# Optimization experiments

Measured on AMD Instinct MI355X. Metric: run time of the kernel, lower is better.

Reference implementation:

```python
import jax, jax.numpy as jnp
import numpy as np
from jax import lax

ANCHOR_NUM = 5
OUTPUT_NUM = 4  # 'reg' branch


def setup_inputs() -> dict:
    key = jax.random.key(0)
    k1, k2 = jax.random.split(key)
    detection = jax.random.normal(k1, (64, 20, 20, 256), dtype=jnp.float32)
    templates = jax.random.normal(k2, (64, 4, 4, 256 * ANCHOR_NUM * OUTPUT_NUM), dtype=jnp.float32)
    return {"detection": detection, "templates": templates}


def reference(detection, templates):
    # detection: [B, Hd, Wd, C]; templates: [B, Hk, Wk, C * O]
    # Original TF code fakes per-example-kernel conv via one big depthwise_conv2d
    # followed by reduce_sum over channel groups. Mathematically:
    #   out[b, y, x, o] = sum_{i,j,c} detection[b, y+i, x+j, c] * tmpl[b, i, j, c, o]
    # i.e. a per-example VALID cross-correlation. We express it as a vmapped conv.
    B, Hd, Wd, C = detection.shape
    _, Hk, Wk, CO = templates.shape
    O = CO // C  # anchor_num * output_num = 20
    tmpl = templates.reshape(B, Hk, Wk, C, O)

    def corr_one(det, ker):
        # det: [Hd, Wd, C], ker: [Hk, Wk, C, O] -> [Ho, Wo, O]
        out = lax.conv_general_dilated(
            det[None],  # [1, Hd, Wd, C]
            ker,        # HWIO
            window_strides=(1, 1),
            padding="VALID",
            dimension_numbers=("NHWC", "HWIO", "NHWC"),
        )
        return out[0]

    out = jax.vmap(corr_one)(detection, tmpl)  # [B, Ho, Wo, O]
    return out
```

## Files before the change

### kernel.cpp

```cpp
#include <hip/hip_runtime.h>
#include <hip/hip_bf16.h>


typedef __bf16 bf16x8 __attribute__((ext_vector_type(8)));
typedef float f32x4 __attribute__((ext_vector_type(4)));

#define NB 64
#define C_TOT 256
#define CQ 32
#define NQ 8
#define NPOS 400
#define NP 289
#define NO 20
#define OPAD 24
#define PTILE (NP * NO)
#define DET_LDS_BYTES (NPOS * CQ * 2)
#define TMP_LDS_BYTES (16 * OPAD * CQ * 2)

__device__ __forceinline__ unsigned short bfbits(float f) {
  __bf16 h = (__bf16)f;
  return __builtin_bit_cast(unsigned short, h);
}

__global__ __launch_bounds__(256)
void reduce_kernel(const float4* __restrict__ ws, float4* __restrict__ out, int n4) {
  int i = blockIdx.x * 256 + threadIdx.x;
  if (i >= n4) return;
  float4 s = ws[i];
  #pragma unroll
  for (int q = 1; q < NQ; ++q) {
    float4 v = ws[q * n4 + i];
    s.x += v.x; s.y += v.y; s.z += v.z; s.w += v.w;
  }
  out[i] = s;
}

__device__ __forceinline__ void det_write(char* detB, int it, float4 v) {
  int pos = it >> 3, cg = it & 7;
  unsigned long long pk =
      (unsigned long long)bfbits(v.x) |
      ((unsigned long long)bfbits(v.y) << 16) |
      ((unsigned long long)bfbits(v.z) << 32) |
      ((unsigned long long)bfbits(v.w) << 48);
  int byte = pos * 64 + (((cg >> 1) ^ ((pos >> 1) & 3)) << 4) + (cg & 1) * 8;
  *(unsigned long long*)(detB + byte) = pk;
}

__global__ __launch_bounds__(256, 3)
void siamese_kernel(const float* __restrict__ det,
                    const float* __restrict__ tmp,
                    float* __restrict__ ws) {
  __shared__ alignas(16) char lds[DET_LDS_BYTES + TMP_LDS_BYTES];
  char* detB = lds;
  char* tmpB = lds + DET_LDS_BYTES;

  const int tid = threadIdx.x;
  const int b   = blockIdx.x >> 3;
  const int q   = blockIdx.x & 7;
  const int c0  = q * CQ;

  const float* __restrict__ dsrc = det + (size_t)b * (NPOS * C_TOT) + c0;
  const float* __restrict__ tsrc = tmp + (size_t)b * (16 * C_TOT * NO);

  {
    float4 v[6];
    #pragma unroll
    for (int k = 0; k < 6; ++k) {
      int it = tid + k * 256;
      v[k] = *(const float4*)(dsrc + (it >> 3) * C_TOT + (it & 7) * 4);
    }
    #pragma unroll
    for (int k = 0; k < 6; ++k) det_write(detB, tid + k * 256, v[k]);
    #pragma unroll
    for (int k = 0; k < 6; ++k) {
      int it = tid + (k + 6) * 256;
      v[k] = *(const float4*)(dsrc + (it >> 3) * C_TOT + (it & 7) * 4);
    }
    float4 vt;
    if (tid < 128) {
      int it = 3072 + tid;
      vt = *(const float4*)(dsrc + (it >> 3) * C_TOT + (it & 7) * 4);
    }
    #pragma unroll
    for (int k = 0; k < 6; ++k) det_write(detB, tid + (k + 6) * 256, v[k]);
    if (tid < 128) det_write(detB, 3072 + tid, vt);
  }

  {
    #pragma unroll
    for (int pp = 0; pp < 2; ++pp) {
      int pr = tid + pp * 256;
      int ij = pr >> 5, c = pr & 31;
      const float* s = tsrc + ij * (C_TOT * NO) + (c0 + c) * NO;
      float4 u[5];
      #pragma unroll
      for (int k = 0; k < 5; ++k) u[k] = *(const float4*)(s + k * 4);
      unsigned short sv[20];
      #pragma unroll
      for (int k = 0; k < 5; ++k) {
        sv[k*4+0] = bfbits(u[k].x); sv[k*4+1] = bfbits(u[k].y);
        sv[k*4+2] = bfbits(u[k].z); sv[k*4+3] = bfbits(u[k].w);
      }
      char* base = tmpB + ij * (OPAD * 64) + (c & 7) * 2;
      int g = (c >> 3) << 4;
      #pragma unroll
      for (int o = 0; o < NO; ++o) {
        int byte = o * 64 + (g ^ (((o >> 1) & 3) << 4));
        *(unsigned short*)(base + byte) = sv[o];
      }
    }
  }

  __syncthreads();

  const int w    = tid >> 6;
  const int lane = tid & 63;
  const int lo   = lane & 15;
  const int hi   = lane >> 4;
  const int nm   = (w < 3) ? 5 : 4;

  int posb[5];
  #pragma unroll
  for (int mi = 0; mi < 5; ++mi) {
    int m = w + mi * 4;
    int p = m * 16 + lo;
    if (p > NP - 1) p = NP - 1;
    posb[mi] = (p / 17) * 20 + (p % 17);
  }

  f32x4 acc[5][2] = {};

  const int o0r  = lo;
  const int o1r  = (16 + lo < OPAD) ? (16 + lo) : (OPAD - 1);
  const int bad0 = o0r * 64 + ((hi ^ ((o0r >> 1) & 3)) << 4);
  const int bad1 = o1r * 64 + ((hi ^ ((o1r >> 1) & 3)) << 4);

  for (int ij = 0; ij < 16; ++ij) {
    const int sh = (ij >> 2) * 20 + (ij & 3);

    bf16x8 bf0 = *(const bf16x8*)(tmpB + bad0 + ij * (OPAD * 64));
    bf16x8 bf1 = *(const bf16x8*)(tmpB + bad1 + ij * (OPAD * 64));

    #pragma unroll
    for (int mi = 0; mi < 5; ++mi) {
      if (mi < nm) {
        int pos  = posb[mi] + sh;
        int byte = pos * 64 + ((hi ^ ((pos >> 1) & 3)) << 4);
        bf16x8 a = *(const bf16x8*)(detB + byte);
        acc[mi][0] = __builtin_amdgcn_mfma_f32_16x16x32_bf16(a, bf0, acc[mi][0], 0, 0, 0);
        acc[mi][1] = __builtin_amdgcn_mfma_f32_16x16x32_bf16(a, bf1, acc[mi][1], 0, 0, 0);
      }
    }
  }

  float* __restrict__ pws = ws + ((size_t)q * NB + b) * PTILE;
  #pragma unroll
  for (int mi = 0; mi < 5; ++mi) {
    if (mi < nm) {
      int m = w + mi * 4;
      #pragma unroll
      for (int n = 0; n < 2; ++n) {
        int o = n * 16 + lo;
        if (o < NO) {
          #pragma unroll
          for (int v = 0; v < 4; ++v) {
            int p = m * 16 + hi * 4 + v;
            if (p < NP) pws[p * NO + o] = acc[mi][n][v];
          }
        }
      }
    }
  }
}

extern "C" void kernel_launch(void* const* d_in, const int* in_sizes, int n_in,
                              void* d_out, int out_size, void* d_ws, size_t ws_size,
                              hipStream_t stream) {
  (void)in_sizes; (void)n_in; (void)ws_size;
  const float* det = (const float*)d_in[0];
  const float* tmp = (const float*)d_in[1];
  float* out = (float*)d_out;
  float* ws  = (float*)d_ws;

  siamese_kernel<<<dim3(NB * NQ), dim3(256), 0, stream>>>(det, tmp, ws);
  int n4 = out_size / 4;
  reduce_kernel<<<dim3((n4 + 255) / 256), dim3(256), 0, stream>>>(
      (const float4*)ws, (float4*)out, n4);
}
```

Measured before the change: 23.09 us.

## Use 512-thread blocks, transposed workspace layout, and LDS-transposing reduction kernel

The main kernel now runs 512 threads per block (8 waves) and gives each wave fewer M tiles. It rewrites the detection and template staging to use 16-byte global loads and 16-byte LDS stores. Partial results go to the workspace in an o-major layout padded to 292 positions, so each thread writes one float4 instead of four scalars. The reduce kernel sums the eight channel-quarter partials per block and transposes through shared memory back to the [p, o] output layout. The cost is lower occupancy per thread and an extra LDS pass in the reduction.

```diff
diff --git a/kernel.cpp b/kernel.cpp
--- a/kernel.cpp
+++ b/kernel.cpp
@@ -11,9 +11,9 @@
 #define NQ 8
 #define NPOS 400
 #define NP 289
+#define NPP 292
 #define NO 20
 #define OPAD 24
-#define PTILE (NP * NO)
 #define DET_LDS_BYTES (NPOS * CQ * 2)
 #define TMP_LDS_BYTES (16 * OPAD * CQ * 2)
 
@@ -21,32 +21,48 @@
   __bf16 h = (__bf16)f;
   return __builtin_bit_cast(unsigned short, h);
 }
+__device__ __forceinline__ unsigned pk2(float a, float b) {
+  return (unsigned)bfbits(a) | ((unsigned)bfbits(b) << 16);
+}
 
 __global__ __launch_bounds__(256)
-void reduce_kernel(const float4* __restrict__ ws, float4* __restrict__ out, int n4) {
-  int i = blockIdx.x * 256 + threadIdx.x;
-  if (i >= n4) return;
-  float4 s = ws[i];
-  #pragma unroll
-  for (int q = 1; q < NQ; ++q) {
-    float4 v = ws[q * n4 + i];
-    s.x += v.x; s.y += v.y; s.z += v.z; s.w += v.w;
-  }
-  out[i] = s;
-}
-
-__device__ __forceinline__ void det_write(char* detB, int it, float4 v) {
-  int pos = it >> 3, cg = it & 7;
-  unsigned long long pk =
-      (unsigned long long)bfbits(v.x) |
-      ((unsigned long long)bfbits(v.y) << 16) |
-      ((unsigned long long)bfbits(v.z) << 32) |
-      ((unsigned long long)bfbits(v.w) << 48);
-  int byte = pos * 64 + (((cg >> 1) ^ ((pos >> 1) & 3)) << 4) + (cg & 1) * 8;
-  *(unsigned long long*)(detB + byte) = pk;
-}
-
-__global__ __launch_bounds__(256, 3)
+void reduce_kernel(const float* __restrict__ ws, float* __restrict__ out) {
+  __shared__ float sbuf[NO * 80];
+  const int b   = blockIdx.x >> 2;
+  const int pg  = blockIdx.x & 3;
+  const int p0g = pg * 80;
+  const int np  = (NP - p0g < 80) ? (NP - p0g) : 80;
+  const int nq4 = (np + 3) >> 2;
+
+  const int units = NO * nq4;
+  for (int t = threadIdx.x; t < units; t += 256) {
+    int o  = t / nq4;
+    int pq = t - o * nq4;
+    int pp = p0g + pq * 4;
+    const float* src = ws + ((size_t)b * NO + o) * NPP + pp;
+    f32x4 s = *(const f32x4*)src;
+    #pragma unroll
+    for (int q = 1; q < NQ; ++q) {
+      f32x4 v = *(const f32x4*)(src + (size_t)q * (NB * NO * NPP));
+      s += v;
+    }
+    *(f32x4*)(&sbuf[o * 80 + pq * 4]) = s;
+  }
+  __syncthreads();
+
+  for (int p = threadIdx.x; p < np; p += 256) {
+    float* dst = out + (size_t)b * (NP * NO) + (p0g + p) * NO;
+    #pragma unroll
+    for (int k = 0; k < 5; ++k) {
+      f32x4 v;
+      #pragma unroll
+      for (int j = 0; j < 4; ++j) v[j] = sbuf[(k * 4 + j) * 80 + p];
+      *(f32x4*)(dst + k * 4) = v;
+    }
+  }
+}
+
+__global__ __launch_bounds__(512, 2)
 void siamese_kernel(const float* __restrict__ det,
                     const float* __restrict__ tmp,
                     float* __restrict__ ws) {
@@ -63,51 +79,48 @@
   const float* __restrict__ tsrc = tmp + (size_t)b * (16 * C_TOT * NO);
 
   {
-    float4 v[6];
-    #pragma unroll
-    for (int k = 0; k < 6; ++k) {
-      int it = tid + k * 256;
-      v[k] = *(const float4*)(dsrc + (it >> 3) * C_TOT + (it & 7) * 4);
-    }
-    #pragma unroll
-    for (int k = 0; k < 6; ++k) det_write(detB, tid + k * 256, v[k]);
-    #pragma unroll
-    for (int k = 0; k < 6; ++k) {
-      int it = tid + (k + 6) * 256;
-      v[k] = *(const float4*)(dsrc + (it >> 3) * C_TOT + (it & 7) * 4);
-    }
-    float4 vt;
-    if (tid < 128) {
-      int it = 3072 + tid;
-      vt = *(const float4*)(dsrc + (it >> 3) * C_TOT + (it & 7) * 4);
-    }
-    #pragma unroll
-    for (int k = 0; k < 6; ++k) det_write(detB, tid + (k + 6) * 256, v[k]);
-    if (tid < 128) det_write(detB, 3072 + tid, vt);
-  }
-
-  {
-    #pragma unroll
-    for (int pp = 0; pp < 2; ++pp) {
-      int pr = tid + pp * 256;
-      int ij = pr >> 5, c = pr & 31;
-      const float* s = tsrc + ij * (C_TOT * NO) + (c0 + c) * NO;
-      float4 u[5];
-      #pragma unroll
-      for (int k = 0; k < 5; ++k) u[k] = *(const float4*)(s + k * 4);
-      unsigned short sv[20];
-      #pragma unroll
-      for (int k = 0; k < 5; ++k) {
-        sv[k*4+0] = bfbits(u[k].x); sv[k*4+1] = bfbits(u[k].y);
-        sv[k*4+2] = bfbits(u[k].z); sv[k*4+3] = bfbits(u[k].w);
-      }
-      char* base = tmpB + ij * (OPAD * 64) + (c & 7) * 2;
-      int g = (c >> 3) << 4;
-      #pragma unroll
-      for (int o = 0; o < NO; ++o) {
-        int byte = o * 64 + (g ^ (((o >> 1) & 3) << 4));
-        *(unsigned short*)(base + byte) = sv[o];
-      }
+    #pragma unroll
+    for (int k = 0; k < 3; ++k) {
+      int u   = tid + k * 512;
+      int pos = u >> 2, cp = u & 3;
+      const float* s = dsrc + pos * C_TOT + cp * 8;
+      float4 A = *(const float4*)s;
+      float4 B = *(const float4*)(s + 4);
+      uint4 w = { pk2(A.x, A.y), pk2(A.z, A.w), pk2(B.x, B.y), pk2(B.z, B.w) };
+      *(uint4*)(detB + pos * 64 + ((cp ^ ((pos >> 1) & 3)) << 4)) = w;
+    }
+    if (tid < 64) {
+      int u   = 1536 + tid;
+      int pos = u >> 2, cp = u & 3;
+      const float* s = dsrc + pos * C_TOT + cp * 8;
+      float4 A = *(const float4*)s;
+      float4 B = *(const float4*)(s + 4);
+      uint4 w = { pk2(A.x, A.y), pk2(A.z, A.w), pk2(B.x, B.y), pk2(B.z, B.w) };
+      *(uint4*)(detB + pos * 64 + ((cp ^ ((pos >> 1) & 3)) << 4)) = w;
+    }
+  }
+
+  if (tid < 320) {
+    int ij = tid / 20;
+    int r  = tid - ij * 20;
+    int co = r / 5;
+    int oq = r - co * 5;
+    const float* s = tsrc + ij * (C_TOT * NO) + (c0 + co * 8) * NO + oq * 4;
+    float4 v[8];
+    #pragma unroll
+    for (int rr = 0; rr < 8; ++rr) v[rr] = *(const float4*)(s + rr * NO);
+    char* base = tmpB + ij * (OPAD * 64);
+    #pragma unroll
+    for (int k = 0; k < 4; ++k) {
+      int o = oq * 4 + k;
+      uint4 w;
+      #define COMP(V) ((k == 0) ? (V).x : (k == 1) ? (V).y : (k == 2) ? (V).z : (V).w)
+      w.x = pk2(COMP(v[0]), COMP(v[1]));
+      w.y = pk2(COMP(v[2]), COMP(v[3]));
+      w.z = pk2(COMP(v[4]), COMP(v[5]));
+      w.w = pk2(COMP(v[6]), COMP(v[7]));
+      #undef COMP
+      *(uint4*)(base + o * 64 + ((co ^ ((o >> 1) & 3)) << 4)) = w;
     }
   }
 
@@ -117,18 +130,18 @@
   const int lane = tid & 63;
   const int lo   = lane & 15;
   const int hi   = lane >> 4;
-  const int nm   = (w < 3) ? 5 : 4;
-
-  int posb[5];
+  const int nm   = (w < 3) ? 3 : 2;
+
+  int posb[3];
   #pragma unroll
-  for (int mi = 0; mi < 5; ++mi) {
-    int m = w + mi * 4;
+  for (int mi = 0; mi < 3; ++mi) {
+    int m = w + mi * 8;
     int p = m * 16 + lo;
     if (p > NP - 1) p = NP - 1;
     posb[mi] = (p / 17) * 20 + (p % 17);
   }
 
-  f32x4 acc[5][2] = {};
+  f32x4 acc[3][2] = {};
 
   const int o0r  = lo;
   const int o1r  = (16 + lo < OPAD) ? (16 + lo) : (OPAD - 1);
@@ -142,7 +155,7 @@
     bf16x8 bf1 = *(const bf16x8*)(tmpB + bad1 + ij * (OPAD * 64));
 
     #pragma unroll
-    for (int mi = 0; mi < 5; ++mi) {
+    for (int mi = 0; mi < 3; ++mi) {
       if (mi < nm) {
         int pos  = posb[mi] + sh;
         int byte = pos * 64 + ((hi ^ ((pos >> 1) & 3)) << 4);
@@ -153,19 +166,21 @@
     }
   }
 
-  float* __restrict__ pws = ws + ((size_t)q * NB + b) * PTILE;
+  float* __restrict__ pws = ws + ((size_t)q * NB + b) * (NO * NPP);
   #pragma unroll
-  for (int mi = 0; mi < 5; ++mi) {
+  for (int mi = 0; mi < 3; ++mi) {
     if (mi < nm) {
-      int m = w + mi * 4;
+      int p0 = (w + mi * 8) * 16 + hi * 4;
       #pragma unroll
       for (int n = 0; n < 2; ++n) {
         int o = n * 16 + lo;
         if (o < NO) {
-          #pragma unroll
-          for (int v = 0; v < 4; ++v) {
-            int p = m * 16 + hi * 4 + v;
-            if (p < NP) pws[p * NO + o] = acc[mi][n][v];
+          if (p0 + 4 <= NP) {
+            *(f32x4*)(pws + o * NPP + p0) = acc[mi][n];
+          } else if (p0 < NP) {
+            #pragma unroll
+            for (int v = 0; v < 4; ++v)
+              if (p0 + v < NP) pws[o * NPP + p0 + v] = acc[mi][n][v];
           }
         }
       }
@@ -176,14 +191,12 @@
 extern "C" void kernel_launch(void* const* d_in, const int* in_sizes, int n_in,
                               void* d_out, int out_size, void* d_ws, size_t ws_size,
                               hipStream_t stream) {
-  (void)in_sizes; (void)n_in; (void)ws_size;
+  (void)in_sizes; (void)n_in; (void)out_size; (void)ws_size;
   const float* det = (const float*)d_in[0];
   const float* tmp = (const float*)d_in[1];
   float* out = (float*)d_out;
   float* ws  = (float*)d_ws;
 
-  siamese_kernel<<<dim3(NB * NQ), dim3(256), 0, stream>>>(det, tmp, ws);
-  int n4 = out_size / 4;
-  reduce_kernel<<<dim3((n4 + 255) / 256), dim3(256), 0, stream>>>(
-      (const float4*)ws, (float4*)out, n4);
-}
+  siamese_kernel<<<dim3(NB * NQ), dim3(512), 0, stream>>>(det, tmp, ws);
+  reduce_kernel<<<dim3(NB * 4), dim3(256), 0, stream>>>(ws, out);
+}
```

New measurement: 22.80 us. No clear change (-1.2%).
